# Kernel tuning notes

Hardware: AMD Instinct MI355X
Metric: run time of the kernel (lower is better)

Reference implementation:

```python
import jax, jax.numpy as jnp
import numpy as np

N_ITEMS = 100000
N_EDGES = 800000
D = 64
N_LAYERS = 3  # config['ii_layers']


def setup_inputs() -> dict:
    key = jax.random.key(0)
    k1, k2, k3, k4 = jax.random.split(key, 4)
    rows = jax.random.randint(k1, (N_EDGES,), 0, N_ITEMS, dtype=jnp.int64 if jax.config.jax_enable_x64 else jnp.int32)
    cols = jax.random.randint(k2, (N_EDGES,), 0, N_ITEMS, dtype=jnp.int64 if jax.config.jax_enable_x64 else jnp.int32)
    vals = jax.random.uniform(k3, (N_EDGES,), dtype=jnp.float32)
    item_embeddings = jax.random.normal(k4, (N_ITEMS, D), dtype=jnp.float32)
    return {"rows": rows, "cols": cols, "vals": vals, "item_embeddings": item_embeddings}


def _spmm(rows, cols, vals, x):
    # sparse.mm(A, x) with A in COO: out[r] += vals[e] * x[c] for each edge e=(r,c)
    msgs = vals[:, None] * x[cols]            # [E, D] gathered & weighted messages
    return jax.ops.segment_sum(msgs, rows, num_segments=N_ITEMS)


def reference(rows, cols, vals, item_embeddings):
    # HyperConv: iterate SpMM, average initial + all layer outputs (fused running sum).
    acc = item_embeddings
    cur = item_embeddings
    for _ in range(N_LAYERS):
        cur = _spmm(rows, cols, vals, cur)
        acc = acc + cur
    return acc / jnp.asarray(N_LAYERS + 1, dtype=item_embeddings.dtype)
```

## Files before the change

### kernel.cpp

```cpp
#include <hip/hip_runtime.h>
#include <hip/hip_fp16.h>


#define NI 100000
#define NE 800000
#define DD 64

#define RPB  128
#define BINS ((NI + RPB - 1) / RPB)
#define EPB  1024
#define P1B  ((NE + EPB - 1) / EPB)
#define CAP  1536
#define BC   32
#define CVB  6250

typedef int   i4 __attribute__((ext_vector_type(4)));
typedef float f4 __attribute__((ext_vector_type(4)));

static __device__ __forceinline__ float2 h2f(int w) {
    __half2 h = *(__half2*)&w;
    return __half22float2(h);
}

__global__ __launch_bounds__(256) void part1_conv_k(const int* __restrict__ rows,
                                                    const int* __restrict__ cols,
                                                    const float* __restrict__ vals,
                                                    int* __restrict__ bin_cnt,
                                                    int2* __restrict__ binned,
                                                    const float4* __restrict__ x,
                                                    __half* __restrict__ xh,
                                                    int n4) {
    int t = threadIdx.x;
    if (blockIdx.x >= P1B) {
        int i = (blockIdx.x - P1B) * 256 + t;
        if (i < n4) {
            float4 v = x[i];
            __half2* dst = (__half2*)(xh + (size_t)i * 4);
            dst[0] = __floats2half2_rn(v.x, v.y);
            dst[1] = __floats2half2_rn(v.z, v.w);
        }
        return;
    }
    __shared__ int hist[BINS], base[BINS], cur[BINS];
    for (int i = t; i < BINS; i += 256) hist[i] = 0;
    __syncthreads();
    int e0 = blockIdx.x * EPB;
    for (int i = t; i < EPB; i += 256) {
        int e = e0 + i;
        if (e < NE) atomicAdd(&hist[rows[e] >> 7], 1);
    }
    __syncthreads();
    for (int i = t; i < BINS; i += 256) {
        int c = hist[i];
        base[i] = c ? atomicAdd(&bin_cnt[i], c) : 0;
        cur[i] = 0;
    }
    __syncthreads();
    for (int i = t; i < EPB; i += 256) {
        int e = e0 + i;
        if (e < NE) {
            int r = rows[e];
            int b = r >> 7;
            int pos = base[b] + atomicAdd(&cur[b], 1);
            if (pos < CAP)
                binned[(size_t)b * CAP + pos] =
                    make_int2(((r & 127) << 17) | cols[e], __float_as_int(vals[e]));
        }
    }
}

__global__ __launch_bounds__(256) void part2_k(const int* __restrict__ bin_cnt,
                                               const int2* __restrict__ binned,
                                               int2* __restrict__ bucket,
                                               int* __restrict__ fill) {
    __shared__ int cur[RPB];
    int t = threadIdx.x;
    int b = blockIdx.x;
    for (int i = t; i < RPB; i += 256) cur[i] = 0;
    __syncthreads();
    int cnt = bin_cnt[b];
    if (cnt > CAP) cnt = CAP;
    const int2* src = binned + (size_t)b * CAP;
    for (int i = t; i < cnt; i += 256) {
        int2 e = src[i];
        int rl = e.x >> 17;
        int pos = atomicAdd(&cur[rl], 1);
        if (pos < BC)
            bucket[((size_t)b * RPB + rl) * BC + pos] = make_int2(e.x & 0x1FFFF, e.y);
    }
    __syncthreads();
    for (int i = t; i < RPB; i += 256) {
        int r = b * RPB + i;
        if (r < NI) {
            int c = (cur[i] < BC) ? cur[i] : BC;
            if (c & 1) {
                bucket[((size_t)b * RPB + i) * BC + c] = make_int2(0, 0);
                c++;
            }
            fill[r] = c;
        }
    }
}

template <int MODE>
__global__ __launch_bounds__(256, 8) void spmm_k(const int* __restrict__ fill,
                                                 const int2* __restrict__ bucket,
                                                 const __half* __restrict__ xin,
                                                 __half* __restrict__ nxt,
                                                 const float* __restrict__ x0,
                                                 const __half* __restrict__ s1,
                                                 float* __restrict__ outp) {
    int tid  = threadIdx.x;
    int lane = tid & 63;
    int grp  = lane >> 3;
    int ll   = lane & 7;
    int r    = blockIdx.x * 32 + (tid >> 6) * 8 + grp;
    int deg  = fill[r];
    const int2* ep = bucket + (size_t)r * BC;

    int wmax = deg;
    wmax = max(wmax, __shfl_xor(wmax, 8, 64));
    wmax = max(wmax, __shfl_xor(wmax, 16, 64));
    wmax = max(wmax, __shfl_xor(wmax, 32, 64));
    int wmax4 = (wmax + 3) & ~3;

    i4 q0 = (i4)0, q1 = (i4)0;
    if (2 * ll < deg)      q0 = __builtin_nontemporal_load((const i4*)(ep + 2 * ll));
    if (16 + 2 * ll < deg) q1 = __builtin_nontemporal_load((const i4*)(ep + 16 + 2 * ll));

    float a0 = 0.f, a1 = 0.f, a2 = 0.f, a3 = 0.f;
    float a4 = 0.f, a5 = 0.f, a6 = 0.f, a7 = 0.f;

    for (int j = 0; j < wmax4; j += 4) {
        int s0 = (lane & 56) | ((j >> 1) & 7);
        int s1i = s0 + 1;
        i4 qa = (j < 16) ? q0 : q1;
        int c0  = __shfl(qa[0], s0, 64);
        int v0i = __shfl(qa[1], s0, 64);
        int c1  = __shfl(qa[2], s0, 64);
        int v1i = __shfl(qa[3], s0, 64);
        int c2  = __shfl(qa[0], s1i, 64);
        int v2i = __shfl(qa[1], s1i, 64);
        int c3  = __shfl(qa[2], s1i, 64);
        int v3i = __shfl(qa[3], s1i, 64);

        i4 g0 = *(const i4*)(xin + (size_t)c0 * DD + 8 * ll);
        i4 g1 = *(const i4*)(xin + (size_t)c1 * DD + 8 * ll);
        i4 g2 = *(const i4*)(xin + (size_t)c2 * DD + 8 * ll);
        i4 g3 = *(const i4*)(xin + (size_t)c3 * DD + 8 * ll);

        float v0 = __int_as_float(v0i);
        float v1 = __int_as_float(v1i);
        float v2 = __int_as_float(v2i);
        float v3 = __int_as_float(v3i);
        float2 f;
        f = h2f(g0[0]); a0 += v0 * f.x; a1 += v0 * f.y;
        f = h2f(g0[1]); a2 += v0 * f.x; a3 += v0 * f.y;
        f = h2f(g0[2]); a4 += v0 * f.x; a5 += v0 * f.y;
        f = h2f(g0[3]); a6 += v0 * f.x; a7 += v0 * f.y;
        f = h2f(g1[0]); a0 += v1 * f.x; a1 += v1 * f.y;
        f = h2f(g1[1]); a2 += v1 * f.x; a3 += v1 * f.y;
        f = h2f(g1[2]); a4 += v1 * f.x; a5 += v1 * f.y;
        f = h2f(g1[3]); a6 += v1 * f.x; a7 += v1 * f.y;
        f = h2f(g2[0]); a0 += v2 * f.x; a1 += v2 * f.y;
        f = h2f(g2[1]); a2 += v2 * f.x; a3 += v2 * f.y;
        f = h2f(g2[2]); a4 += v2 * f.x; a5 += v2 * f.y;
        f = h2f(g2[3]); a6 += v2 * f.x; a7 += v2 * f.y;
        f = h2f(g3[0]); a0 += v3 * f.x; a1 += v3 * f.y;
        f = h2f(g3[1]); a2 += v3 * f.x; a3 += v3 * f.y;
        f = h2f(g3[2]); a4 += v3 * f.x; a5 += v3 * f.y;
        f = h2f(g3[3]); a6 += v3 * f.x; a7 += v3 * f.y;
    }

    if (MODE == 2) {
        size_t fo = (size_t)r * DD + 8 * ll;
        f4 xa = __builtin_nontemporal_load((const f4*)(x0 + fo));
        f4 xb = __builtin_nontemporal_load((const f4*)(x0 + fo) + 1);
        i4 s1u = __builtin_nontemporal_load((const i4*)(s1 + fo));
        i4 s2u = *(const i4*)(xin + fo);
        f4 oa, ob;
        float2 f1, f2;
        f1 = h2f(s1u[0]); f2 = h2f(s2u[0]);
        oa[0] = (xa[0] + f1.x + f2.x + a0) * 0.25f;
        oa[1] = (xa[1] + f1.y + f2.y + a1) * 0.25f;
        f1 = h2f(s1u[1]); f2 = h2f(s2u[1]);
        oa[2] = (xa[2] + f1.x + f2.x + a2) * 0.25f;
        oa[3] = (xa[3] + f1.y + f2.y + a3) * 0.25f;
        f1 = h2f(s1u[2]); f2 = h2f(s2u[2]);
        ob[0] = (xb[0] + f1.x + f2.x + a4) * 0.25f;
        ob[1] = (xb[1] + f1.y + f2.y + a5) * 0.25f;
        f1 = h2f(s1u[3]); f2 = h2f(s2u[3]);
        ob[2] = (xb[2] + f1.x + f2.x + a6) * 0.25f;
        ob[3] = (xb[3] + f1.y + f2.y + a7) * 0.25f;
        f4* op = (f4*)(outp + fo);
        __builtin_nontemporal_store(oa, op);
        __builtin_nontemporal_store(ob, op + 1);
    } else {
        i4 o;
        __half2 h;
        h = __floats2half2_rn(a0, a1); o[0] = *(int*)&h;
        h = __floats2half2_rn(a2, a3); o[1] = *(int*)&h;
        h = __floats2half2_rn(a4, a5); o[2] = *(int*)&h;
        h = __floats2half2_rn(a6, a7); o[3] = *(int*)&h;
        *(i4*)(nxt + (size_t)r * DD + 8 * ll) = o;
    }
}

#define NB ((NI + 255) / 256)

__global__ __launch_bounds__(256) void init_k(const float4* __restrict__ x,
                                              float4* __restrict__ cur,
                                              float4* __restrict__ acc, int n4) {
    int i = blockIdx.x * 256 + threadIdx.x;
    if (i < n4) { float4 v = x[i]; cur[i] = v; acc[i] = v; }
}

__global__ __launch_bounds__(256) void hist_k(const int* __restrict__ rows,
                                              int* __restrict__ counts) {
    int e = blockIdx.x * 256 + threadIdx.x;
    if (e < NE) atomicAdd(&counts[rows[e]], 1);
}

__global__ __launch_bounds__(256) void scan1_k(const int* __restrict__ counts,
                                               int* __restrict__ bsum) {
    __shared__ int s[256];
    int t = threadIdx.x;
    int i = blockIdx.x * 256 + t;
    s[t] = (i < NI) ? counts[i] : 0;
    __syncthreads();
    for (int off = 128; off > 0; off >>= 1) {
        if (t < off) s[t] += s[t + off];
        __syncthreads();
    }
    if (t == 0) bsum[blockIdx.x] = s[0];
}

__global__ __launch_bounds__(512) void scan2_k(int* __restrict__ bsum) {
    __shared__ int s[512];
    int t = threadIdx.x;
    int v = (t < NB) ? bsum[t] : 0;
    s[t] = v;
    __syncthreads();
    for (int off = 1; off < 512; off <<= 1) {
        int tmp = (t >= off) ? s[t - off] : 0;
        __syncthreads();
        s[t] += tmp;
        __syncthreads();
    }
    if (t < NB) bsum[t] = s[t] - v;
}

__global__ __launch_bounds__(256) void scan3_k(const int* __restrict__ counts,
                                               const int* __restrict__ bsum,
                                               int* __restrict__ rowptr) {
    __shared__ int s[256];
    int t = threadIdx.x;
    int i = blockIdx.x * 256 + t;
    int v = (i < NI) ? counts[i] : 0;
    s[t] = v;
    __syncthreads();
    for (int off = 1; off < 256; off <<= 1) {
        int tmp = (t >= off) ? s[t - off] : 0;
        __syncthreads();
        s[t] += tmp;
        __syncthreads();
    }
    int excl = s[t] - v + bsum[blockIdx.x];
    if (i < NI) rowptr[i] = excl;
    if (i == NI - 1) rowptr[NI] = excl + v;
}

__global__ __launch_bounds__(256) void scatter_k(const int* __restrict__ rows,
                                                 const int* __restrict__ cols,
                                                 const float* __restrict__ vals,
                                                 const int* __restrict__ rowptr,
                                                 int* __restrict__ fillc,
                                                 int2* __restrict__ edges) {
    int e = blockIdx.x * 256 + threadIdx.x;
    if (e < NE) {
        int r = rows[e];
        int pos = rowptr[r] + atomicAdd(&fillc[r], 1);
        edges[pos] = make_int2(cols[e], __float_as_int(vals[e]));
    }
}

__global__ __launch_bounds__(256) void spmm_csr_k(const int* __restrict__ rowptr,
                                                  const int2* __restrict__ edges,
                                                  const float* __restrict__ x,
                                                  float* __restrict__ nxt,
                                                  float* __restrict__ acc,
                                                  int last) {
    int r = __builtin_amdgcn_readfirstlane(blockIdx.x * 4 + (threadIdx.x >> 6));
    int lane = threadIdx.x & 63;
    int beg = rowptr[r];
    int end = rowptr[r + 1];
    float s = 0.f;
    int j = beg;
    for (; j + 3 < end; j += 4) {
        int2 e0 = edges[j], e1 = edges[j + 1], e2 = edges[j + 2], e3 = edges[j + 3];
        float g0 = x[(size_t)e0.x * DD + lane];
        float g1 = x[(size_t)e1.x * DD + lane];
        float g2 = x[(size_t)e2.x * DD + lane];
        float g3 = x[(size_t)e3.x * DD + lane];
        s += __int_as_float(e0.y) * g0; s += __int_as_float(e1.y) * g1;
        s += __int_as_float(e2.y) * g2; s += __int_as_float(e3.y) * g3;
    }
    for (; j < end; ++j) {
        int2 e = edges[j];
        s += __int_as_float(e.y) * x[(size_t)e.x * DD + lane];
    }
    size_t o = (size_t)r * DD + lane;
    if (last) acc[o] = (acc[o] + s) * 0.25f;
    else { nxt[o] = s; acc[o] += s; }
}

extern "C" void kernel_launch(void* const* d_in, const int* in_sizes, int n_in,
                              void* d_out, int out_size, void* d_ws, size_t ws_size,
                              hipStream_t stream) {
    const int*   rows = (const int*)d_in[0];
    const int*   cols = (const int*)d_in[1];
    const float* vals = (const float*)d_in[2];
    const float* x    = (const float*)d_in[3];
    float* outp = (float*)d_out;

    const size_t fbuf  = (size_t)NI * DD * sizeof(float);
    const size_t hbuf  = (size_t)NI * DD * sizeof(__half);
    const int    n4        = NI * DD / 4;
    const int    grid_elem = (n4 + 255) / 256;

    char* wsp = (char*)d_ws;

    size_t off_xh     = 0;
    size_t off_s1     = off_xh + hbuf;
    size_t off_s2     = off_s1 + hbuf;
    size_t off_bucket = off_s2 + hbuf;
    size_t off_binned = off_bucket + (size_t)NI * BC * 8;
    size_t off_fill   = off_binned + (size_t)BINS * CAP * 8;
    size_t off_bcnt   = off_fill + (size_t)NI * 4;
    size_t need       = off_bcnt + (size_t)BINS * 4;

    if (ws_size >= need) {
        __half* xh      = (__half*)(wsp + off_xh);
        __half* s1h     = (__half*)(wsp + off_s1);
        __half* s2h     = (__half*)(wsp + off_s2);
        int2*   bucket  = (int2*)(wsp + off_bucket);
        int2*   binned  = (int2*)(wsp + off_binned);
        int*    fill    = (int*)(wsp + off_fill);
        int*    bin_cnt = (int*)(wsp + off_bcnt);

        hipMemsetAsync(bin_cnt, 0, BINS * sizeof(int), stream);
        part1_conv_k<<<P1B + CVB, 256, 0, stream>>>(rows, cols, vals, bin_cnt, binned,
                                                    (const float4*)x, xh, n4);
        part2_k<<<BINS, 256, 0, stream>>>(bin_cnt, binned, bucket, fill);

        const int grid_spmm = NI / 32;
        spmm_k<0><<<grid_spmm, 256, 0, stream>>>(fill, bucket, xh,  s1h, nullptr, nullptr, nullptr);
        spmm_k<1><<<grid_spmm, 256, 0, stream>>>(fill, bucket, s1h, s2h, nullptr, nullptr, nullptr);
        spmm_k<2><<<grid_spmm, 256, 0, stream>>>(fill, bucket, s2h, nullptr, x, s1h, outp);
        return;
    }

    const int grid_edge = (NE + 255) / 256;
    const int grid_csr  = NI / 4;

    float* bufA   = (float*)wsp;
    float* bufB   = (float*)(wsp + fbuf);
    int2*  edges  = (int2*)(wsp + 2 * fbuf);
    int*   rowptr = (int*)(wsp + 2 * fbuf + (size_t)NE * 8);
    int*   counts = rowptr + (NI + 1);
    int*   bsum   = counts + NI;

    hipMemsetAsync(counts, 0, NI * sizeof(int), stream);
    hist_k<<<grid_edge, 256, 0, stream>>>(rows, counts);
    scan1_k<<<NB, 256, 0, stream>>>(counts, bsum);
    scan2_k<<<1, 512, 0, stream>>>(bsum);
    scan3_k<<<NB, 256, 0, stream>>>(counts, bsum, rowptr);
    hipMemsetAsync(counts, 0, NI * sizeof(int), stream);
    scatter_k<<<grid_edge, 256, 0, stream>>>(rows, cols, vals, rowptr, counts, edges);
    init_k<<<grid_elem, 256, 0, stream>>>((const float4*)x, (float4*)bufA,
                                          (float4*)outp, n4);
    spmm_csr_k<<<grid_csr, 256, 0, stream>>>(rowptr, edges, bufA, bufB, outp, 0);
    spmm_csr_k<<<grid_csr, 256, 0, stream>>>(rowptr, edges, bufB, bufA, outp, 0);
    spmm_csr_k<<<grid_csr, 256, 0, stream>>>(rowptr, edges, bufA, bufB, outp, 1);
}
```

Measured before the change: 187.0 us.

## Stage edges in shared memory by bin for coalesced writes; split bucket pass

The first binning pass now uses coarser 512-row bins. Each block prefix-scans its local histogram, stages its edges in shared memory sorted by bin, and then writes each bin's run contiguously to global memory instead of scattering one edge at a time. The second pass launches four blocks per coarse bin. Each block rescans the whole bin but keeps only its quarter of the rows, so parallelism stays the same with fewer bins. The cost is four reads of each bin in the second pass and more shared memory per block in the first pass.

After: 170.9 us (median of 2 runs). 8.6% less time.

```diff
diff --git a/kernel.cpp b/kernel.cpp
--- a/kernel.cpp
+++ b/kernel.cpp
@@ -6,13 +6,15 @@
 #define NE 800000
 #define DD 64
 
-#define RPB  128
+#define RPB  512
 #define BINS ((NI + RPB - 1) / RPB)
-#define EPB  1024
+#define EPB  2048
 #define P1B  ((NE + EPB - 1) / EPB)
-#define CAP  1536
+#define CAP  5120
 #define BC   32
 #define CVB  6250
+#define SPLIT 4
+#define RQ   (RPB / SPLIT)
 
 typedef int   i4 __attribute__((ext_vector_type(4)));
 typedef float f4 __attribute__((ext_vector_type(4)));
@@ -41,31 +43,53 @@
         }
         return;
     }
-    __shared__ int hist[BINS], base[BINS], cur[BINS];
-    for (int i = t; i < BINS; i += 256) hist[i] = 0;
-    __syncthreads();
-    int e0 = blockIdx.x * EPB;
-    for (int i = t; i < EPB; i += 256) {
-        int e = e0 + i;
-        if (e < NE) atomicAdd(&hist[rows[e] >> 7], 1);
-    }
-    __syncthreads();
-    for (int i = t; i < BINS; i += 256) {
-        int c = hist[i];
-        base[i] = c ? atomicAdd(&bin_cnt[i], c) : 0;
-        cur[i] = 0;
-    }
-    __syncthreads();
-    for (int i = t; i < EPB; i += 256) {
-        int e = e0 + i;
-        if (e < NE) {
-            int r = rows[e];
-            int b = r >> 7;
-            int pos = base[b] + atomicAdd(&cur[b], 1);
-            if (pos < CAP)
-                binned[(size_t)b * CAP + pos] =
-                    make_int2(((r & 127) << 17) | cols[e], __float_as_int(vals[e]));
-        }
+
+    __shared__ int  hist[BINS];
+    __shared__ int  offs[BINS];
+    __shared__ int  base[BINS];
+    __shared__ int  cur[BINS];
+    __shared__ int  sc[256];
+    __shared__ int2 stage[EPB];
+    __shared__ unsigned char sbin[EPB];
+
+    int e0   = blockIdx.x * EPB;
+    int ecnt = NE - e0; if (ecnt > EPB) ecnt = EPB;
+
+    for (int i = t; i < BINS; i += 256) { hist[i] = 0; cur[i] = 0; }
+    __syncthreads();
+    for (int i = t; i < ecnt; i += 256)
+        atomicAdd(&hist[rows[e0 + i] >> 9], 1);
+    __syncthreads();
+
+    int hv = (t < BINS) ? hist[t] : 0;
+    sc[t] = hv;
+    __syncthreads();
+    for (int off = 1; off < 256; off <<= 1) {
+        int xv = (t >= off) ? sc[t - off] : 0;
+        __syncthreads();
+        sc[t] += xv;
+        __syncthreads();
+    }
+    if (t < BINS) {
+        offs[t] = sc[t] - hv;
+        base[t] = hv ? atomicAdd(&bin_cnt[t], hv) : 0;
+    }
+    __syncthreads();
+
+    for (int i = t; i < ecnt; i += 256) {
+        int r = rows[e0 + i];
+        int b = r >> 9;
+        int p = offs[b] + atomicAdd(&cur[b], 1);
+        stage[p] = make_int2(((r & 511) << 17) | cols[e0 + i],
+                             __float_as_int(vals[e0 + i]));
+        sbin[p] = (unsigned char)b;
+    }
+    __syncthreads();
+
+    for (int i = t; i < ecnt; i += 256) {
+        int b   = sbin[i];
+        int pos = base[b] + (i - offs[b]);
+        if (pos < CAP) binned[(size_t)b * CAP + pos] = stage[i];
     }
 }
 
@@ -73,28 +97,33 @@
                                                const int2* __restrict__ binned,
                                                int2* __restrict__ bucket,
                                                int* __restrict__ fill) {
-    __shared__ int cur[RPB];
-    int t = threadIdx.x;
-    int b = blockIdx.x;
-    for (int i = t; i < RPB; i += 256) cur[i] = 0;
-    __syncthreads();
-    int cnt = bin_cnt[b];
+    __shared__ int cur[RQ];
+    int t  = threadIdx.x;
+    int bb = blockIdx.x >> 2;
+    int q  = blockIdx.x & 3;
+    for (int i = t; i < RQ; i += 256) cur[i] = 0;
+    __syncthreads();
+    int cnt = bin_cnt[bb];
     if (cnt > CAP) cnt = CAP;
-    const int2* src = binned + (size_t)b * CAP;
+    const int2* src = binned + (size_t)bb * CAP;
     for (int i = t; i < cnt; i += 256) {
         int2 e = src[i];
         int rl = e.x >> 17;
-        int pos = atomicAdd(&cur[rl], 1);
-        if (pos < BC)
-            bucket[((size_t)b * RPB + rl) * BC + pos] = make_int2(e.x & 0x1FFFF, e.y);
-    }
-    __syncthreads();
-    for (int i = t; i < RPB; i += 256) {
-        int r = b * RPB + i;
+        if ((rl >> 7) == q) {
+            int pos = atomicAdd(&cur[rl & (RQ - 1)], 1);
+            if (pos < BC)
+                bucket[((size_t)bb * RPB + rl) * BC + pos] =
+                    make_int2(e.x & 0x1FFFF, e.y);
+        }
+    }
+    __syncthreads();
+    for (int i = t; i < RQ; i += 256) {
+        int rl = q * RQ + i;
+        int r  = bb * RPB + rl;
         if (r < NI) {
             int c = (cur[i] < BC) ? cur[i] : BC;
             if (c & 1) {
-                bucket[((size_t)b * RPB + i) * BC + c] = make_int2(0, 0);
+                bucket[((size_t)bb * RPB + rl) * BC + c] = make_int2(0, 0);
                 c++;
             }
             fill[r] = c;
@@ -351,7 +380,7 @@
         hipMemsetAsync(bin_cnt, 0, BINS * sizeof(int), stream);
         part1_conv_k<<<P1B + CVB, 256, 0, stream>>>(rows, cols, vals, bin_cnt, binned,
                                                     (const float4*)x, xh, n4);
-        part2_k<<<BINS, 256, 0, stream>>>(bin_cnt, binned, bucket, fill);
+        part2_k<<<BINS * SPLIT, 256, 0, stream>>>(bin_cnt, binned, bucket, fill);
 
         const int grid_spmm = NI / 32;
         spmm_k<0><<<grid_spmm, 256, 0, stream>>>(fill, bucket, xh,  s1h, nullptr, nullptr, nullptr);
```
